# Optimization experiments

Measured on AMD Instinct MI355X. Metric: run time of the kernel, lower is better.

## Reference

```python
import jax, jax.numpy as jnp
import numpy as np

F = 64      # input_v_size
E = 64      # emb_v_size
H = 8       # int(sqrt(emb_v_size))
P = 512     # proj_e_size
B, T = 64, 256


def setup_inputs() -> dict:
    key = jax.random.key(0)
    ks = jax.random.split(key, 14)
    s1 = 1.0            # Linear(1->H): fan_in=1
    s2 = 1.0 / np.sqrt(H)
    s3 = 1.0 / np.sqrt(F * E)
    return {
        "x":    jax.random.normal(ks[0], (B, T, F), dtype=jnp.float32),
        "time": jax.random.uniform(ks[1], (B, T, F), dtype=jnp.float32),
        # stacked per-feature Linear(1->H): weight [F,H], bias [F,H]
        "w1v": jax.random.uniform(ks[2], (F, H), jnp.float32, -s1, s1),
        "b1v": jax.random.uniform(ks[3], (F, H), jnp.float32, -s1, s1),
        # stacked per-feature Linear(H->E, bias=False): [F,H,E]
        "w2v": jax.random.uniform(ks[4], (F, H, E), jnp.float32, -s2, s2),
        "w1t": jax.random.uniform(ks[5], (F, H), jnp.float32, -s1, s1),
        "b1t": jax.random.uniform(ks[6], (F, H), jnp.float32, -s1, s1),
        "w2t": jax.random.uniform(ks[7], (F, H, E), jnp.float32, -s2, s2),
        # Wx, Wt: Linear(F*E -> P) stored as [F*E, P] (= torch weight.T)
        "wx":  jax.random.uniform(ks[8], (F * E, P), jnp.float32, -s3, s3),
        "bx":  jax.random.uniform(ks[9], (P,), jnp.float32, -s3, s3),
        "wt":  jax.random.uniform(ks[10], (F * E, P), jnp.float32, -s3, s3),
        "bt":  jax.random.uniform(ks[11], (P,), jnp.float32, -s3, s3),
    }


def _branch(inp, w1, b1, w2):
    # inp [B,T,F]; w1,b1 [F,H]; w2 [F,H,E]
    h = jnp.tanh(inp[..., None] * w1 + b1)          # [B,T,F,H]
    e = jnp.einsum("btfh,fhe->btfe", h, w2)          # [B,T,F,E]
    return e.reshape(*inp.shape[:2], -1)              # [B,T,F*E]


def reference(x, time, w1v, b1v, w2v, w1t, b1t, w2t, wx, bx, wt, bt):
    x_out = _branch(x, w1v, b1v, w2v)
    t_out = _branch(time, w1t, b1t, w2t)
    return (x_out @ wx + bx) + (t_out @ wt + bt)      # [B,T,P]
```

## Files before the change

### kernel.cpp

```cpp
#include <hip/hip_runtime.h>
#include <cstdint>
#include <cstddef>

#define FF 64
#define EE 64
#define HH 8
#define PP 512
#define MM 16384
#define KK 1024

typedef __bf16 bf16x8 __attribute__((ext_vector_type(8)));
typedef float  floatx4 __attribute__((ext_vector_type(4)));

__device__ __forceinline__ unsigned short f2bf(float f) {
    unsigned int u = __float_as_uint(f);
    u += 0x7FFFu + ((u >> 16) & 1u);
    return (unsigned short)(u >> 16);
}

__device__ __forceinline__ unsigned pack2(unsigned short a, unsigned short b) {
    return (unsigned)a | ((unsigned)b << 16);
}

__device__ __forceinline__ void gl_lds16(const unsigned short* g, unsigned short* s) {
    __builtin_amdgcn_global_load_lds(
        (__attribute__((address_space(1))) void*)(void*)g,
        (__attribute__((address_space(3))) void*)s,
        16, 0, 0);
}

__global__ __launch_bounds__(256) void combine_kernel(
    const float* __restrict__ w2v, const float* __restrict__ w2t,
    const float* __restrict__ wx,  const float* __restrict__ wt,
    unsigned short* __restrict__ BmatT)
{
    const int br = blockIdx.x >> 6;
    const int f  = blockIdx.x & 63;
    const float* __restrict__ w2 = br ? w2t : w2v;
    const float* __restrict__ W  = br ? wt  : wx;
    __shared__ float w2s[HH * EE];
    const int tid = threadIdx.x;
    for (int i = tid; i < HH * EE; i += 256) w2s[i] = w2[f * HH * EE + i];
    __syncthreads();

    float acc0[HH] = {0,0,0,0,0,0,0,0};
    float acc1[HH] = {0,0,0,0,0,0,0,0};
    const float* Wrow = W + (size_t)f * EE * PP;
    for (int e = 0; e < EE; ++e) {
        const float wv0 = Wrow[(size_t)e * PP + tid];
        const float wv1 = Wrow[(size_t)e * PP + tid + 256];
        #pragma unroll
        for (int h = 0; h < HH; ++h) {
            const float c = w2s[h * EE + e];
            acc0[h] = __builtin_fmaf(c, wv0, acc0[h]);
            acc1[h] = __builtin_fmaf(c, wv1, acc1[h]);
        }
    }
    const int kbase = br * 512 + f * 8;
    uint4 v0, v1;
    v0.x = pack2(f2bf(acc0[0]), f2bf(acc0[1]));
    v0.y = pack2(f2bf(acc0[2]), f2bf(acc0[3]));
    v0.z = pack2(f2bf(acc0[4]), f2bf(acc0[5]));
    v0.w = pack2(f2bf(acc0[6]), f2bf(acc0[7]));
    v1.x = pack2(f2bf(acc1[0]), f2bf(acc1[1]));
    v1.y = pack2(f2bf(acc1[2]), f2bf(acc1[3]));
    v1.z = pack2(f2bf(acc1[4]), f2bf(acc1[5]));
    v1.w = pack2(f2bf(acc1[6]), f2bf(acc1[7]));
    *reinterpret_cast<uint4*>(&BmatT[(size_t)tid        * KK + kbase]) = v0;
    *reinterpret_cast<uint4*>(&BmatT[(size_t)(tid+256)  * KK + kbase]) = v1;
}

__global__ __launch_bounds__(256) void hfeat_kernel(
    const float* __restrict__ x,   const float* __restrict__ tmv,
    const float* __restrict__ w1v, const float* __restrict__ b1v,
    const float* __restrict__ w1t, const float* __restrict__ b1t,
    unsigned short* __restrict__ Hc)
{
    const int g   = blockIdx.x * 256 + threadIdx.x;
    const int row = g >> 7;
    const int j   = g & 127;
    const int br  = j >> 6;
    const int f   = j & 63;
    const float val = br ? tmv[(size_t)row * FF + f] : x[(size_t)row * FF + f];
    const float* w1 = br ? w1t : w1v;
    const float* b1 = br ? b1t : b1v;
    const float4 wa = reinterpret_cast<const float4*>(w1)[f * 2];
    const float4 wb = reinterpret_cast<const float4*>(w1)[f * 2 + 1];
    const float4 ba = reinterpret_cast<const float4*>(b1)[f * 2];
    const float4 bb = reinterpret_cast<const float4*>(b1)[f * 2 + 1];
    float hv[8];
    hv[0] = tanhf(__builtin_fmaf(val, wa.x, ba.x));
    hv[1] = tanhf(__builtin_fmaf(val, wa.y, ba.y));
    hv[2] = tanhf(__builtin_fmaf(val, wa.z, ba.z));
    hv[3] = tanhf(__builtin_fmaf(val, wa.w, ba.w));
    hv[4] = tanhf(__builtin_fmaf(val, wb.x, bb.x));
    hv[5] = tanhf(__builtin_fmaf(val, wb.y, bb.y));
    hv[6] = tanhf(__builtin_fmaf(val, wb.z, bb.z));
    hv[7] = tanhf(__builtin_fmaf(val, wb.w, bb.w));
    uint4 v;
    v.x = pack2(f2bf(hv[0]), f2bf(hv[1]));
    v.y = pack2(f2bf(hv[2]), f2bf(hv[3]));
    v.z = pack2(f2bf(hv[4]), f2bf(hv[5]));
    v.w = pack2(f2bf(hv[6]), f2bf(hv[7]));
    *reinterpret_cast<uint4*>(&Hc[(size_t)row * KK + br * 512 + f * 8]) = v;
}

__global__ __launch_bounds__(256) void gemm_kernel(
    const unsigned short* __restrict__ A,
    const unsigned short* __restrict__ Bt,
    const float* __restrict__ bx, const float* __restrict__ bt,
    float* __restrict__ out)
{
    __shared__ unsigned short As[128 * 64];
    __shared__ unsigned short Bs[128 * 64];
    const int tid  = threadIdx.x;
    const int wave = tid >> 6;
    const int lane = tid & 63;
    const int m0 = blockIdx.y * 128;
    const int n0 = blockIdx.x * 128;
    const int wr = wave >> 1;
    const int wc = wave & 1;
    const int q  = lane >> 4;
    const int ml = lane & 15;
    const int lr = lane >> 3;
    const int lk = (lane & 7) * 8;

    floatx4 acc[4][4];
    #pragma unroll
    for (int i = 0; i < 4; ++i)
        #pragma unroll
        for (int j = 0; j < 4; ++j)
            acc[i][j] = (floatx4){0.f, 0.f, 0.f, 0.f};

    for (int k0 = 0; k0 < KK; k0 += 64) {
        #pragma unroll
        for (int i = 0; i < 4; ++i) {
            const int seg = wave * 4 + i;
            const int r = seg * 8 + lr;
            gl_lds16(&A [(size_t)(m0 + r) * KK + k0 + lk], &As[seg * 512]);
            gl_lds16(&Bt[(size_t)(n0 + r) * KK + k0 + lk], &Bs[seg * 512]);
        }
        __syncthreads();
        #pragma unroll
        for (int kk = 0; kk < 64; kk += 32) {
            bf16x8 af[4], bfr[4];
            #pragma unroll
            for (int mt = 0; mt < 4; ++mt)
                af[mt] = *reinterpret_cast<const bf16x8*>(
                    &As[(wr * 64 + mt * 16 + ml) * 64 + kk + q * 8]);
            #pragma unroll
            for (int nt = 0; nt < 4; ++nt)
                bfr[nt] = *reinterpret_cast<const bf16x8*>(
                    &Bs[(wc * 64 + nt * 16 + ml) * 64 + kk + q * 8]);
            #pragma unroll
            for (int mt = 0; mt < 4; ++mt)
                #pragma unroll
                for (int nt = 0; nt < 4; ++nt)
                    acc[mt][nt] = __builtin_amdgcn_mfma_f32_16x16x32_bf16(
                        af[mt], bfr[nt], acc[mt][nt], 0, 0, 0);
        }
        __syncthreads();
    }

    #pragma unroll
    for (int nt = 0; nt < 4; ++nt) {
        const int n = n0 + wc * 64 + nt * 16 + ml;
        const float bias = bx[n] + bt[n];
        #pragma unroll
        for (int mt = 0; mt < 4; ++mt) {
            const int mb = m0 + wr * 64 + mt * 16 + q * 4;
            #pragma unroll
            for (int r = 0; r < 4; ++r)
                out[(size_t)(mb + r) * PP + n] = acc[mt][nt][r] + bias;
        }
    }
}

extern "C" void kernel_launch(void* const* d_in, const int* in_sizes, int n_in,
                              void* d_out, int out_size, void* d_ws, size_t ws_size,
                              hipStream_t stream)
{
    const float* x   = (const float*)d_in[0];
    const float* tmv = (const float*)d_in[1];
    const float* w1v = (const float*)d_in[2];
    const float* b1v = (const float*)d_in[3];
    const float* w2v = (const float*)d_in[4];
    const float* w1t = (const float*)d_in[5];
    const float* b1t = (const float*)d_in[6];
    const float* w2t = (const float*)d_in[7];
    const float* wx  = (const float*)d_in[8];
    const float* bx  = (const float*)d_in[9];
    const float* wt  = (const float*)d_in[10];
    const float* bt  = (const float*)d_in[11];
    float* out = (float*)d_out;

    unsigned short* Bws = (unsigned short*)d_ws;
    unsigned short* Hws = (unsigned short*)((char*)d_ws + (1u << 20));

    combine_kernel<<<128, 256, 0, stream>>>(w2v, w2t, wx, wt, Bws);
    hfeat_kernel<<<MM * KK / 8 / 256, 256, 0, stream>>>(x, tmv, w1v, b1v, w1t, b1t, Hws);
    gemm_kernel<<<dim3(PP / 128, MM / 128), 256, 0, stream>>>(Hws, Bws, bx, bt, out);
}
```

Baseline: 141.8 us.

## Fuse prep kernels, use fast tanh, swizzle LDS, reorder GEMM grid

Merges the weight-combine and hidden-feature kernels into one launch, and splits the combine work across twice as many blocks so they run alongside the feature blocks. It replaces tanhf with an exp/rcp approximation built from hardware instructions. In the GEMM it applies an XOR swizzle to the LDS layout to avoid bank conflicts, and swaps grid axes so consecutive blocks share B tiles. The fast tanh lowers accuracy slightly, though the result is rounded to bf16 anyway.

Measured after the change: 127.3 us. 1.11x faster.

```diff
diff --git a/kernel.cpp b/kernel.cpp
--- a/kernel.cpp
+++ b/kernel.cpp
@@ -22,6 +22,14 @@
     return (unsigned)a | ((unsigned)b << 16);
 }
 
+__device__ __forceinline__ float fast_tanh(float x) {
+    float e, r;
+    asm("v_exp_f32 %0, %1" : "=v"(e) : "v"(x * 2.8853900817779268f));
+    float d = e + 1.0f;
+    asm("v_rcp_f32 %0, %1" : "=v"(r) : "v"(d));
+    return __builtin_fmaf(-2.0f, r, 1.0f);
+}
+
 __device__ __forceinline__ void gl_lds16(const unsigned short* g, unsigned short* s) {
     __builtin_amdgcn_global_load_lds(
         (__attribute__((address_space(1))) void*)(void*)g,
@@ -29,80 +37,70 @@
         16, 0, 0);
 }
 
-__global__ __launch_bounds__(256) void combine_kernel(
-    const float* __restrict__ w2v, const float* __restrict__ w2t,
-    const float* __restrict__ wx,  const float* __restrict__ wt,
-    unsigned short* __restrict__ BmatT)
-{
-    const int br = blockIdx.x >> 6;
-    const int f  = blockIdx.x & 63;
-    const float* __restrict__ w2 = br ? w2t : w2v;
-    const float* __restrict__ W  = br ? wt  : wx;
-    __shared__ float w2s[HH * EE];
-    const int tid = threadIdx.x;
-    for (int i = tid; i < HH * EE; i += 256) w2s[i] = w2[f * HH * EE + i];
-    __syncthreads();
-
-    float acc0[HH] = {0,0,0,0,0,0,0,0};
-    float acc1[HH] = {0,0,0,0,0,0,0,0};
-    const float* Wrow = W + (size_t)f * EE * PP;
-    for (int e = 0; e < EE; ++e) {
-        const float wv0 = Wrow[(size_t)e * PP + tid];
-        const float wv1 = Wrow[(size_t)e * PP + tid + 256];
-        #pragma unroll
-        for (int h = 0; h < HH; ++h) {
-            const float c = w2s[h * EE + e];
-            acc0[h] = __builtin_fmaf(c, wv0, acc0[h]);
-            acc1[h] = __builtin_fmaf(c, wv1, acc1[h]);
-        }
-    }
-    const int kbase = br * 512 + f * 8;
-    uint4 v0, v1;
-    v0.x = pack2(f2bf(acc0[0]), f2bf(acc0[1]));
-    v0.y = pack2(f2bf(acc0[2]), f2bf(acc0[3]));
-    v0.z = pack2(f2bf(acc0[4]), f2bf(acc0[5]));
-    v0.w = pack2(f2bf(acc0[6]), f2bf(acc0[7]));
-    v1.x = pack2(f2bf(acc1[0]), f2bf(acc1[1]));
-    v1.y = pack2(f2bf(acc1[2]), f2bf(acc1[3]));
-    v1.z = pack2(f2bf(acc1[4]), f2bf(acc1[5]));
-    v1.w = pack2(f2bf(acc1[6]), f2bf(acc1[7]));
-    *reinterpret_cast<uint4*>(&BmatT[(size_t)tid        * KK + kbase]) = v0;
-    *reinterpret_cast<uint4*>(&BmatT[(size_t)(tid+256)  * KK + kbase]) = v1;
-}
-
-__global__ __launch_bounds__(256) void hfeat_kernel(
+__global__ __launch_bounds__(256) void prep_kernel(
     const float* __restrict__ x,   const float* __restrict__ tmv,
     const float* __restrict__ w1v, const float* __restrict__ b1v,
     const float* __restrict__ w1t, const float* __restrict__ b1t,
-    unsigned short* __restrict__ Hc)
+    const float* __restrict__ w2v, const float* __restrict__ w2t,
+    const float* __restrict__ wx,  const float* __restrict__ wt,
+    unsigned short* __restrict__ BmatT, unsigned short* __restrict__ Hc)
 {
-    const int g   = blockIdx.x * 256 + threadIdx.x;
-    const int row = g >> 7;
-    const int j   = g & 127;
-    const int br  = j >> 6;
-    const int f   = j & 63;
-    const float val = br ? tmv[(size_t)row * FF + f] : x[(size_t)row * FF + f];
-    const float* w1 = br ? w1t : w1v;
-    const float* b1 = br ? b1t : b1v;
-    const float4 wa = reinterpret_cast<const float4*>(w1)[f * 2];
-    const float4 wb = reinterpret_cast<const float4*>(w1)[f * 2 + 1];
-    const float4 ba = reinterpret_cast<const float4*>(b1)[f * 2];
-    const float4 bb = reinterpret_cast<const float4*>(b1)[f * 2 + 1];
-    float hv[8];
-    hv[0] = tanhf(__builtin_fmaf(val, wa.x, ba.x));
-    hv[1] = tanhf(__builtin_fmaf(val, wa.y, ba.y));
-    hv[2] = tanhf(__builtin_fmaf(val, wa.z, ba.z));
-    hv[3] = tanhf(__builtin_fmaf(val, wa.w, ba.w));
-    hv[4] = tanhf(__builtin_fmaf(val, wb.x, bb.x));
-    hv[5] = tanhf(__builtin_fmaf(val, wb.y, bb.y));
-    hv[6] = tanhf(__builtin_fmaf(val, wb.z, bb.z));
-    hv[7] = tanhf(__builtin_fmaf(val, wb.w, bb.w));
-    uint4 v;
-    v.x = pack2(f2bf(hv[0]), f2bf(hv[1]));
-    v.y = pack2(f2bf(hv[2]), f2bf(hv[3]));
-    v.z = pack2(f2bf(hv[4]), f2bf(hv[5]));
-    v.w = pack2(f2bf(hv[6]), f2bf(hv[7]));
-    *reinterpret_cast<uint4*>(&Hc[(size_t)row * KK + br * 512 + f * 8]) = v;
+    const int tid = threadIdx.x;
+    if (blockIdx.x < 256) {
+        const int bid = blockIdx.x;
+        const int br = bid >> 7;
+        const int f  = (bid >> 1) & 63;
+        const int nh = bid & 1;
+        const float* __restrict__ w2 = br ? w2t : w2v;
+        const float* __restrict__ W  = br ? wt  : wx;
+        __shared__ float w2s[HH * EE];
+        for (int i = tid; i < HH * EE; i += 256) w2s[i] = w2[f * HH * EE + i];
+        __syncthreads();
+        const int n = nh * 256 + tid;
+        float acc[HH] = {0,0,0,0,0,0,0,0};
+        const float* Wcol = W + (size_t)f * EE * PP + n;
+        #pragma unroll 8
+        for (int e = 0; e < EE; ++e) {
+            const float wv = Wcol[(size_t)e * PP];
+            #pragma unroll
+            for (int h = 0; h < HH; ++h)
+                acc[h] = __builtin_fmaf(w2s[h * EE + e], wv, acc[h]);
+        }
+        uint4 v;
+        v.x = pack2(f2bf(acc[0]), f2bf(acc[1]));
+        v.y = pack2(f2bf(acc[2]), f2bf(acc[3]));
+        v.z = pack2(f2bf(acc[4]), f2bf(acc[5]));
+        v.w = pack2(f2bf(acc[6]), f2bf(acc[7]));
+        *reinterpret_cast<uint4*>(&BmatT[(size_t)n * KK + br * 512 + f * 8]) = v;
+    } else {
+        const int g   = (blockIdx.x - 256) * 256 + tid;
+        const int row = g >> 7;
+        const int j   = g & 127;
+        const int br  = j >> 6;
+        const int f   = j & 63;
+        const float val = br ? tmv[(size_t)row * FF + f] : x[(size_t)row * FF + f];
+        const float* w1 = br ? w1t : w1v;
+        const float* b1 = br ? b1t : b1v;
+        const float4 wa = reinterpret_cast<const float4*>(w1)[f * 2];
+        const float4 wb = reinterpret_cast<const float4*>(w1)[f * 2 + 1];
+        const float4 ba = reinterpret_cast<const float4*>(b1)[f * 2];
+        const float4 bb = reinterpret_cast<const float4*>(b1)[f * 2 + 1];
+        float hv[8];
+        hv[0] = fast_tanh(__builtin_fmaf(val, wa.x, ba.x));
+        hv[1] = fast_tanh(__builtin_fmaf(val, wa.y, ba.y));
+        hv[2] = fast_tanh(__builtin_fmaf(val, wa.z, ba.z));
+        hv[3] = fast_tanh(__builtin_fmaf(val, wa.w, ba.w));
+        hv[4] = fast_tanh(__builtin_fmaf(val, wb.x, bb.x));
+        hv[5] = fast_tanh(__builtin_fmaf(val, wb.y, bb.y));
+        hv[6] = fast_tanh(__builtin_fmaf(val, wb.z, bb.z));
+        hv[7] = fast_tanh(__builtin_fmaf(val, wb.w, bb.w));
+        uint4 v;
+        v.x = pack2(f2bf(hv[0]), f2bf(hv[1]));
+        v.y = pack2(f2bf(hv[2]), f2bf(hv[3]));
+        v.z = pack2(f2bf(hv[4]), f2bf(hv[5]));
+        v.w = pack2(f2bf(hv[6]), f2bf(hv[7]));
+        *reinterpret_cast<uint4*>(&Hc[(size_t)row * KK + br * 512 + f * 8]) = v;
+    }
 }
 
 __global__ __launch_bounds__(256) void gemm_kernel(
@@ -116,14 +114,15 @@
     const int tid  = threadIdx.x;
     const int wave = tid >> 6;
     const int lane = tid & 63;
-    const int m0 = blockIdx.y * 128;
-    const int n0 = blockIdx.x * 128;
+    const int m0 = blockIdx.x * 128;
+    const int n0 = blockIdx.y * 128;
     const int wr = wave >> 1;
     const int wc = wave & 1;
-    const int q  = lane >> 4;
-    const int ml = lane & 15;
-    const int lr = lane >> 3;
-    const int lk = (lane & 7) * 8;
+    const int q   = lane >> 4;
+    const int ml  = lane & 15;
+    const int mlx = ml & 7;
+    const int lr  = lane >> 3;
+    const int lkg = ((lane & 7) ^ lr) * 8;
 
     floatx4 acc[4][4];
     #pragma unroll
@@ -137,21 +136,23 @@
         for (int i = 0; i < 4; ++i) {
             const int seg = wave * 4 + i;
             const int r = seg * 8 + lr;
-            gl_lds16(&A [(size_t)(m0 + r) * KK + k0 + lk], &As[seg * 512]);
-            gl_lds16(&Bt[(size_t)(n0 + r) * KK + k0 + lk], &Bs[seg * 512]);
+            gl_lds16(&A [(size_t)(m0 + r) * KK + k0 + lkg], &As[seg * 512]);
+            gl_lds16(&Bt[(size_t)(n0 + r) * KK + k0 + lkg], &Bs[seg * 512]);
         }
         __syncthreads();
         #pragma unroll
         for (int kk = 0; kk < 64; kk += 32) {
+            const int cl = (kk >> 3) + q;
+            const int co = (cl ^ mlx) * 8;
             bf16x8 af[4], bfr[4];
             #pragma unroll
             for (int mt = 0; mt < 4; ++mt)
                 af[mt] = *reinterpret_cast<const bf16x8*>(
-                    &As[(wr * 64 + mt * 16 + ml) * 64 + kk + q * 8]);
+                    &As[(wr * 64 + mt * 16 + ml) * 64 + co]);
             #pragma unroll
             for (int nt = 0; nt < 4; ++nt)
                 bfr[nt] = *reinterpret_cast<const bf16x8*>(
-                    &Bs[(wc * 64 + nt * 16 + ml) * 64 + kk + q * 8]);
+                    &Bs[(wc * 64 + nt * 16 + ml) * 64 + co]);
             #pragma unroll
             for (int mt = 0; mt < 4; ++mt)
                 #pragma unroll
@@ -197,7 +198,7 @@
     unsigned short* Bws = (unsigned short*)d_ws;
     unsigned short* Hws = (unsigned short*)((char*)d_ws + (1u << 20));
 
-    combine_kernel<<<128, 256, 0, stream>>>(w2v, w2t, wx, wt, Bws);
-    hfeat_kernel<<<MM * KK / 8 / 256, 256, 0, stream>>>(x, tmv, w1v, b1v, w1t, b1t, Hws);
-    gemm_kernel<<<dim3(PP / 128, MM / 128), 256, 0, stream>>>(Hws, Bws, bx, bt, out);
-}
+    prep_kernel<<<256 + MM * KK / 8 / 256, 256, 0, stream>>>(
+        x, tmv, w1v, b1v, w1t, b1t, w2v, w2t, wx, wt, Bws, Hws);
+    gemm_kernel<<<dim3(MM / 128, PP / 128), 256, 0, stream>>>(Hws, Bws, bx, bt, out);
+}
```
